# Performance work log

Measured on AMD Instinct MI355X. Metric: run time of the kernel, lower is better.

Reference implementation:

```python
import jax, jax.numpy as jnp
import numpy as np

D_MODEL = 768
D_STATE = 16
D_CONV = 4
EXPAND = 2
D_INNER = EXPAND * D_MODEL          # 1536
DT_RANK = max(1, D_MODEL // 16)     # 48
B, L = 2, 2048


def setup_inputs() -> dict:
    key = jax.random.key(0)
    ks = jax.random.split(key, 8)
    rn = lambda k, shape, scale: (jax.random.normal(k, shape, dtype=jnp.float32) * scale)
    A_init = jnp.broadcast_to(jnp.arange(1, D_STATE + 1, dtype=jnp.float32), (D_INNER, D_STATE))
    return {
        "x": rn(ks[0], (B, L, D_MODEL), 1.0),
        "in_proj_w": rn(ks[1], (2 * D_INNER, D_MODEL), 0.02),
        "conv_w": rn(ks[2], (D_INNER, 1, D_CONV), 0.2),
        "conv_b": jnp.zeros((D_INNER,), jnp.float32),
        "x_proj_w": rn(ks[3], (DT_RANK + 2 * D_STATE, D_INNER), 0.02),
        "dt_proj_w": rn(ks[4], (D_INNER, DT_RANK), 0.05),
        "dt_proj_b": rn(ks[5], (D_INNER,), 0.05),
        "A_log": jnp.log(A_init),
        "D_param": jnp.ones((D_INNER,), jnp.float32),
        "out_proj_w": rn(ks[6], (D_MODEL, D_INNER), 0.02),
        "ln_w": jnp.ones((D_MODEL,), jnp.float32),
        "ln_b": jnp.zeros((D_MODEL,), jnp.float32),
    }


def _layernorm(x, w, b, eps=1e-5):
    mu = x.mean(-1, keepdims=True)
    var = ((x - mu) ** 2).mean(-1, keepdims=True)
    return (x - mu) * jax.lax.rsqrt(var + eps) * w + b


def reference(x, in_proj_w, conv_w, conv_b, x_proj_w, dt_proj_w, dt_proj_b,
              A_log, D_param, out_proj_w, ln_w, ln_b):
    residual = x
    xn = _layernorm(x, ln_w, ln_b)
    xz = xn @ in_proj_w.T                      # [B,L,2*D_INNER]
    x_in, z = jnp.split(xz, 2, axis=-1)
    # depthwise causal conv (pad left d_conv-1, matching pad-both-then-slice)
    xc = jax.lax.conv_general_dilated(
        x_in.transpose(0, 2, 1), conv_w, (1,), [(D_CONV - 1, 0)],
        feature_group_count=D_INNER, dimension_numbers=("NCH", "OIH", "NCH"))
    xc = (xc + conv_b[None, :, None]).transpose(0, 2, 1)   # [B,L,D_INNER]
    xc = jax.nn.silu(xc)

    A = -jnp.exp(A_log)                        # [D_INNER, D_STATE]
    x_dbl = xc @ x_proj_w.T                    # [B,L,DT_RANK+2*D_STATE]
    dt, Bm, C = jnp.split(x_dbl, [DT_RANK, DT_RANK + D_STATE], axis=-1)
    delta = jax.nn.softplus(dt @ dt_proj_w.T + dt_proj_b)  # [B,L,D_INNER]
    deltaA = jnp.exp(jnp.einsum("bld,dn->bldn", delta, A))        # [B,L,D,N]
    deltaBx = jnp.einsum("bld,bln,bld->bldn", delta, Bm, xc)      # [B,L,D,N]

    def step(h, ins):
        dA, dBx, c = ins                       # [B,D,N],[B,D,N],[B,N]
        h = dA * h + dBx
        return h, jnp.einsum("bdn,bn->bd", h, c)

    h0 = jnp.zeros((x.shape[0], D_INNER, D_STATE), xc.dtype)
    _, ys = jax.lax.scan(step, h0, (deltaA.swapaxes(0, 1),
                                    deltaBx.swapaxes(0, 1),
                                    C.swapaxes(0, 1)))
    y = ys.swapaxes(0, 1) + xc * D_param       # [B,L,D_INNER]
    y = y * jax.nn.silu(z)
    return y @ out_proj_w.T + residual
```

## Files before the change

### kernel.cpp

```cpp
#include <hip/hip_runtime.h>
#include <hip/hip_bf16.h>
#include <math.h>

namespace {

typedef __hip_bfloat16 bf16;
typedef unsigned short u16;
typedef __bf16 bf8v __attribute__((ext_vector_type(8)));
typedef float f4v __attribute__((ext_vector_type(4)));
typedef short s8v __attribute__((ext_vector_type(8)));
typedef u16 u4v __attribute__((ext_vector_type(4)));

constexpr int Bb = 2;
constexpr int Ll = 2048;
constexpr int DM = 768;
constexpr int DI = 1536;
constexpr int DS = 16;
constexpr int RK = 48;
constexpr int XD = RK + 2 * DS;
constexpr int Mrows = Bb * Ll;
constexpr int NC = 32;
constexpr int CL = Ll / NC;
constexpr float LOG2E = 1.44269504f;

constexpr int NW1 = 2 * DI * DM;
constexpr int NWX = 128 * DI;
constexpr int NWD = DI * 64;
constexpr int NWO = DM * DI;
constexpr int NWC = DI * 4;
constexpr int NWCB = DI;

__device__ inline float b2f(bf16 v) { return __bfloat162float(v); }
__device__ inline bf16 f2b(float v) { return __float2bfloat16(v); }

union BfBits { bf16 h; u16 u; };
__device__ inline u16 f2u(float v) {
  BfBits bb; bb.h = __float2bfloat16(v); return bb.u;
}
__device__ inline float u2f(u16 u) {
  BfBits bb; bb.u = u; return b2f(bb.h);
}

__device__ inline float ldx(const void* p, size_t i, int bf) {
  if (bf) return __bfloat162float(((const bf16*)p)[i]);
  return ((const float*)p)[i];
}

__device__ inline void gload16(const void* g, u16* lds) {
  __builtin_amdgcn_global_load_lds(
      (__attribute__((address_space(1))) void*)g,
      (__attribute__((address_space(3))) void*)lds, 16, 0, 0);
}

__device__ inline int rperm(int d) {
  return (d & 56) | ((d ^ (d >> 3)) & 7);
}

__global__ void detect_kernel(const unsigned int* __restrict__ xw,
                              int* __restrict__ flag) {
  int t = threadIdx.x;
  unsigned int w = xw[t];
  unsigned int lo = w & 0xFFFFu;
  unsigned int ef = (lo >> 7) & 0xFFu;
  bool plaus = (lo == 0u) || (ef >= 104u && ef <= 136u);
  unsigned long long m = __ballot(plaus);
  if (t == 0) flag[0] = (__popcll(m) >= 48) ? 1 : 0;
}

__global__ __launch_bounds__(256) void convert_w1(
    const void* __restrict__ in_proj, const void* __restrict__ x_proj,
    const void* __restrict__ dt_proj, const void* __restrict__ conv_w,
    const void* __restrict__ conv_b,
    bf16* __restrict__ w_in, bf16* __restrict__ w_x, bf16* __restrict__ w_dt,
    bf16* __restrict__ dtA, bf16* __restrict__ w_cv, bf16* __restrict__ w_cb,
    const int* __restrict__ flagp) {
  int bf = flagp[0];
  int e = (blockIdx.x * 256 + threadIdx.x) * 4;
  if (e < NW1) {
    u4v v;
#pragma unroll
    for (int k = 0; k < 4; ++k) v[k] = f2u(ldx(in_proj, e + k, bf));
    *(u4v*)&w_in[e] = v;
    return;
  }
  e -= NW1;
  if (e < NWX) {
    int r = e / DI, c = e % DI;
    u4v v = {};
    if (r < 80) {
#pragma unroll
      for (int k = 0; k < 4; ++k) v[k] = f2u(ldx(x_proj, (size_t)r * DI + c + k, bf));
    }
    *(u4v*)&w_x[e] = v;
    return;
  }
  e -= NWX;
  if (e < NWD) {
    int r = e / 64, c = e % 64;
    u4v v = {};
#pragma unroll
    for (int k = 0; k < 4; ++k)
      if (c + k < RK) v[k] = f2u(ldx(dt_proj, (size_t)r * RK + c + k, bf));
    *(u4v*)&w_dt[e] = v;
    return;
  }
  e -= NWD;
  if (e < Mrows * 16) {
    int row = e / 16, col = RK + (e % 16);
    u4v v = {};
    *(u4v*)&dtA[(size_t)row * 64 + col] = v;
    return;
  }
  e -= Mrows * 16;
  if (e < NWC) {
    u4v v;
#pragma unroll
    for (int k = 0; k < 4; ++k) v[k] = f2u(ldx(conv_w, e + k, bf));
    *(u4v*)&w_cv[e] = v;
    return;
  }
  e -= NWC;
  if (e < NWCB) {
    u4v v;
#pragma unroll
    for (int k = 0; k < 4; ++k) v[k] = f2u(ldx(conv_b, e + k, bf));
    *(u4v*)&w_cb[e] = v;
  }
}

__global__ __launch_bounds__(256) void convert_w2(
    const void* __restrict__ out_proj, bf16* __restrict__ w_out,
    const int* __restrict__ flagp) {
  int bf = flagp[0];
  int e = (blockIdx.x * 256 + threadIdx.x) * 4;
  if (e >= NWO) return;
  u4v v;
#pragma unroll
  for (int k = 0; k < 4; ++k) v[k] = f2u(ldx(out_proj, e + k, bf));
  *(u4v*)&w_out[e] = v;
}

__global__ __launch_bounds__(256) void ln_kernel(
    const void* __restrict__ x, const void* __restrict__ w,
    const void* __restrict__ b, bf16* __restrict__ xn,
    const int* __restrict__ flagp) {
  int bf = flagp[0];
  int row = blockIdx.x;
  int t = threadIdx.x;
  float v[3];
  float s = 0.f, ss = 0.f;
#pragma unroll
  for (int i = 0; i < 3; ++i) {
    v[i] = ldx(x, (size_t)row * DM + t + i * 256, bf);
    s += v[i];
    ss += v[i] * v[i];
  }
#pragma unroll
  for (int off = 32; off; off >>= 1) {
    s += __shfl_down(s, off);
    ss += __shfl_down(ss, off);
  }
  __shared__ float sb[4], ssb[4];
  int wid = t >> 6, lid = t & 63;
  if (lid == 0) { sb[wid] = s; ssb[wid] = ss; }
  __syncthreads();
  if (t == 0) {
    sb[0] = sb[0] + sb[1] + sb[2] + sb[3];
    ssb[0] = ssb[0] + ssb[1] + ssb[2] + ssb[3];
  }
  __syncthreads();
  float mu = sb[0] * (1.f / DM);
  float var = ssb[0] * (1.f / DM) - mu * mu;
  float rs = rsqrtf(var + 1e-5f);
#pragma unroll
  for (int i = 0; i < 3; ++i) {
    int c = t + i * 256;
    xn[(size_t)row * DM + c] =
        f2b((v[i] - mu) * rs * ldx(w, c, bf) + ldx(b, c, bf));
  }
}

template <int EPI, int BM>
__global__ __launch_bounds__(256, 2) void gemm_gl(
    int M, int N, int klen,
    const bf16* __restrict__ A, int lda,
    const bf16* __restrict__ Bw, int ldb,
    void* __restrict__ Cv, void* __restrict__ Cv2, int ldc,
    const void* __restrict__ extra,
    const int* __restrict__ flagp) {
  constexpr int FI = BM / 32;
  __shared__ __align__(16) u16 As[2][BM * 32];
  __shared__ __align__(16) u16 Bs[2][128 * 32];
  int tid = threadIdx.x;
  int l = tid & 63, w = tid >> 6;
  int wr = w >> 1, wc = w & 1;
  int m0 = blockIdx.y * BM, n0 = blockIdx.x * 128;
  int kbeg = blockIdx.z * klen;
  int nt = klen / 64;
  int lr = l & 15, lk = (l >> 4) * 8;
  f4v acc[FI][4] = {};

  int srow = l >> 2, schunk = l & 3;

  for (int t = 0; t < nt; ++t) {
    __syncthreads();
#pragma unroll
    for (int h = 0; h < 2; ++h) {
      int k0 = kbeg + t * 64 + h * 32;
#pragma unroll
      for (int c = 0; c < BM / 64; ++c) {
        int seg = w + c * 4;
        int row = seg * 16 + srow;
        int gcol = k0 + ((schunk ^ ((row >> 1) & 3)) << 3);
        gload16(A + (size_t)(m0 + row) * lda + gcol, &As[h][seg * 512]);
      }
#pragma unroll
      for (int c = 0; c < 2; ++c) {
        int seg = w + c * 4;
        int row = seg * 16 + srow;
        int gcol = k0 + ((schunk ^ ((row >> 1) & 3)) << 3);
        gload16(Bw + (size_t)(n0 + row) * ldb + gcol, &Bs[h][seg * 512]);
      }
    }
    __syncthreads();
#pragma unroll
    for (int h = 0; h < 2; ++h) {
      bf8v af[FI], bfv[4];
#pragma unroll
      for (int i = 0; i < FI; ++i) {
        int row = wr * (BM / 2) + i * 16 + lr;
        af[i] = *(const bf8v*)&As[h][row * 32 + (((lk >> 3) ^ ((row >> 1) & 3)) << 3)];
      }
#pragma unroll
      for (int j = 0; j < 4; ++j) {
        int row = wc * 64 + j * 16 + lr;
        bfv[j] = *(const bf8v*)&Bs[h][row * 32 + (((lk >> 3) ^ ((row >> 1) & 3)) << 3)];
      }
#pragma unroll
      for (int i = 0; i < FI; ++i)
#pragma unroll
        for (int j = 0; j < 4; ++j)
          acc[i][j] = __builtin_amdgcn_mfma_f32_16x16x32_bf16(
              af[i], bfv[j], acc[i][j], 0, 0, 0);
    }
  }

  int bf = flagp[0];
  int lq = l >> 4;
  size_t pbase = (size_t)blockIdx.z * M * ldc;
#pragma unroll
  for (int i = 0; i < FI; ++i) {
#pragma unroll
    for (int j = 0; j < 4; ++j) {
      int nn = n0 + wc * 64 + j * 16 + lr;
      if (nn >= N) continue;
#pragma unroll
      for (int r = 0; r < 4; ++r) {
        int m = m0 + wr * (BM / 2) + i * 16 + lq * 4 + r;
        float v = acc[i][j][r];
        size_t ci = (size_t)m * ldc + nn;
        if (EPI == 0) {
          ((float*)Cv)[pbase + ci] = v;
        } else if (EPI == 1) {
          float tt = v + ldx(extra, nn, bf);
          float sp = (tt > 20.f) ? tt : log1pf(__expf(tt));
          ((bf16*)Cv)[ci] = f2b(sp);
        } else if (EPI == 4) {
          if (nn < DI) ((bf16*)Cv)[(size_t)m * DI + nn] = f2b(v);
          else ((bf16*)Cv2)[(size_t)m * DI + nn - DI] = f2b(v);
        }
      }
    }
  }
}

__global__ __launch_bounds__(256) void reduce_xdbl(
    const float* __restrict__ part, bf16* __restrict__ xdbl,
    bf16* __restrict__ dtA) {
  int idx = blockIdx.x * 256 + threadIdx.x;
  if (idx >= Mrows * XD) return;
  float s = 0.f;
#pragma unroll
  for (int k = 0; k < 8; ++k) s += part[(size_t)k * Mrows * XD + idx];
  bf16 v = f2b(s);
  xdbl[idx] = v;
  int col = idx % XD;
  if (col < RK) dtA[(size_t)(idx / XD) * 64 + col] = v;
}

__global__ __launch_bounds__(256) void reduce_out(
    const float* __restrict__ part, const void* __restrict__ x,
    float* __restrict__ out, const int* __restrict__ flagp) {
  int bf = flagp[0];
  int idx = blockIdx.x * 256 + threadIdx.x;
  if (idx >= Mrows * DM) return;
  out[idx] = part[idx] + part[(size_t)Mrows * DM + idx] + ldx(x, idx, bf);
}

__global__ __launch_bounds__(256) void conv_silu_kernel(
    const bf16* __restrict__ xin, const bf16* __restrict__ w_cv,
    const bf16* __restrict__ w_cb, bf16* __restrict__ xc) {
  int idx = blockIdx.x * 256 + threadIdx.x;
  if (idx >= Mrows * DI / 8) return;
  int d0 = (idx % (DI / 8)) * 8;
  int m = idx / (DI / 8);
  int l = m % Ll;
  s8v wv[4];
#pragma unroll
  for (int q = 0; q < 4; ++q)
    wv[q] = *(const s8v*)(w_cv + (size_t)d0 * 4 + q * 8);
  s8v cbv = *(const s8v*)(w_cb + d0);
  float acc[8];
#pragma unroll
  for (int k = 0; k < 8; ++k) acc[k] = u2f((u16)cbv[k]);
#pragma unroll
  for (int j = 0; j < 4; ++j) {
    int lj = l - 3 + j;
    if (lj < 0) continue;
    s8v xv = *(const s8v*)(xin + (size_t)(m - 3 + j) * DI + d0);
#pragma unroll
    for (int k = 0; k < 8; ++k)
      acc[k] += u2f((u16)wv[(k * 4 + j) >> 3][(k * 4 + j) & 7]) * u2f((u16)xv[k]);
  }
  s8v o;
#pragma unroll
  for (int k = 0; k < 8; ++k) {
    float v = acc[k] / (1.f + __expf(-acc[k]));
    o[k] = (short)f2u(v);
  }
  *(s8v*)(xc + (size_t)m * DI + d0) = o;
}

constexpr int TS = 72;

__global__ __launch_bounds__(256) void scan_p1(
    const bf16* __restrict__ delta, const bf16* __restrict__ xc,
    const bf16* __restrict__ xdbl, const void* __restrict__ A_log,
    float* __restrict__ ca, float* __restrict__ cb,
    const int* __restrict__ flagp) {
  int bf = flagp[0];
  int tid = threadIdx.x;
  int bx = blockIdx.x;
  int b = bx / NC, c = bx % NC;
  int dq = tid >> 2, n4 = tid & 3;
  int d0 = blockIdx.y * 64;
  int d = d0 + dq;
  __shared__ float Bsh[CL * 16];
  __shared__ __align__(16) u16 dT[64 * TS];
  __shared__ __align__(16) u16 xT[64 * TS];
  size_t base = (size_t)b * Ll + c * CL;
  {
    int e = tid * 4;
    int l = e >> 4, n = e & 15;
    size_t row = base + l;
    u4v v = *(const u4v*)((const u16*)xdbl + row * XD + RK + n);
#pragma unroll
    for (int k = 0; k < 4; ++k) Bsh[e + k] = u2f(v[k]);
  }
  {
    int lh = tid >> 3;
    int dd0 = (tid & 7) * 8;
    const u16* dg = (const u16*)delta + (base + 2 * lh) * DI + d0 + dd0;
    const u16* xg = (const u16*)xc + (base + 2 * lh) * DI + d0 + dd0;
    s8v d0v = *(const s8v*)dg;
    s8v d1v = *(const s8v*)(dg + DI);
    s8v x0v = *(const s8v*)xg;
    s8v x1v = *(const s8v*)(xg + DI);
#pragma unroll
    for (int k = 0; k < 8; ++k) {
      int rr = rperm(dd0 + k);
      unsigned int dw = (unsigned int)(u16)d0v[k] |
                        ((unsigned int)(u16)d1v[k] << 16);
      *(unsigned int*)&dT[rr * TS + 2 * lh] = dw;
      dw = (unsigned int)(u16)x0v[k] |
           ((unsigned int)(u16)x1v[k] << 16);
      *(unsigned int*)&xT[rr * TS + 2 * lh] = dw;
    }
  }
  __syncthreads();
  int rq = rperm(dq);
  float An2[4], h[4] = {};
  float sdv = 0.f;
#pragma unroll
  for (int k = 0; k < 4; ++k)
    An2[k] = -__expf(ldx(A_log, (size_t)d * DS + n4 * 4 + k, bf)) * LOG2E;
  for (int l0 = 0; l0 < CL; l0 += 8) {
    s8v dvv = *(const s8v*)&dT[rq * TS + l0];
    s8v xvv = *(const s8v*)&xT[rq * TS + l0];
    float dv[8], xcv[8];
#pragma unroll
    for (int k2 = 0; k2 < 8; ++k2) {
      dv[k2] = u2f((u16)dvv[k2]);
      xcv[k2] = u2f((u16)xvv[k2]);
    }
#pragma unroll
    for (int j = 0; j < 8; ++j) {
      f4v bv = *(const f4v*)&Bsh[(l0 + j) * 16 + n4 * 4];
      float dx = dv[j] * xcv[j];
      sdv += dv[j];
#pragma unroll
      for (int k = 0; k < 4; ++k) {
        float dA = exp2f(dv[j] * An2[k]);
        h[k] = dA * h[k] + dx * bv[k];
      }
    }
  }
  size_t cbase = ((size_t)bx * DI + d) * 16 + n4 * 4;
  f4v av, hv;
#pragma unroll
  for (int k = 0; k < 4; ++k) {
    av[k] = exp2f(sdv * An2[k]);
    hv[k] = h[k];
  }
  *(f4v*)&ca[cbase] = av;
  *(f4v*)&cb[cbase] = hv;
}

__global__ __launch_bounds__(256) void scan_p2(
    const float* __restrict__ ca, float* __restrict__ cb) {
  int tid = threadIdx.x;
  int bx = blockIdx.x;
  int b = bx / (DI / 64);
  int d = (bx % (DI / 64)) * 64 + (tid >> 2);
  int n4 = tid & 3;
  size_t off = (size_t)d * 16 + n4 * 4;
  f4v h = {};
  for (int c = 0; c < NC; ++c) {
    size_t cbase = (size_t)(b * NC + c) * DI * 16 + off;
    f4v av = *(const f4v*)&ca[cbase];
    f4v bv = *(const f4v*)&cb[cbase];
    f4v hv = h;
#pragma unroll
    for (int k = 0; k < 4; ++k) h[k] = av[k] * h[k] + bv[k];
    *(f4v*)&cb[cbase] = hv;
  }
}

__global__ __launch_bounds__(256) void scan_p3(
    bf16* dy, const bf16* __restrict__ xc,
    const bf16* __restrict__ xdbl, const bf16* __restrict__ z,
    const void* __restrict__ A_log, const void* __restrict__ Dp,
    const float* __restrict__ cb, const int* __restrict__ flagp) {
  int bf = flagp[0];
  int tid = threadIdx.x;
  int bx = blockIdx.x;
  int b = bx / NC, c = bx % NC;
  int dq = tid >> 2, n4 = tid & 3;
  int d0 = blockIdx.y * 64;
  int d = d0 + dq;
  __shared__ float BCsh[CL * 32];
  __shared__ __align__(16) u16 dT[64 * TS];
  __shared__ __align__(16) u16 xT[64 * TS];
  size_t base = (size_t)b * Ll + c * CL;
  {
    int e = tid * 8;
    int l = e >> 5, j = e & 31;
    size_t row = base + l;
    s8v v = *(const s8v*)((const u16*)xdbl + row * XD + RK + j);
#pragma unroll
    for (int k = 0; k < 8; ++k) BCsh[e + k] = u2f((u16)v[k]);
  }
  {
    int lh = tid >> 3;
    int dd0 = (tid & 7) * 8;
    const u16* dg = (const u16*)dy + (base + 2 * lh) * DI + d0 + dd0;
    const u16* xg = (const u16*)xc + (base + 2 * lh) * DI + d0 + dd0;
    s8v d0v = *(const s8v*)dg;
    s8v d1v = *(const s8v*)(dg + DI);
    s8v x0v = *(const s8v*)xg;
    s8v x1v = *(const s8v*)(xg + DI);
#pragma unroll
    for (int k = 0; k < 8; ++k) {
      int rr = rperm(dd0 + k);
      unsigned int dw = (unsigned int)(u16)d0v[k] |
                        ((unsigned int)(u16)d1v[k] << 16);
      *(unsigned int*)&dT[rr * TS + 2 * lh] = dw;
      dw = (unsigned int)(u16)x0v[k] |
           ((unsigned int)(u16)x1v[k] << 16);
      *(unsigned int*)&xT[rr * TS + 2 * lh] = dw;
    }
  }
  __syncthreads();
  int rq = rperm(dq);
  float An2[4], h[4];
  size_t cbase = ((size_t)bx * DI + d) * 16 + n4 * 4;
  {
    f4v hv = *(const f4v*)&cb[cbase];
#pragma unroll
    for (int k = 0; k < 4; ++k) h[k] = hv[k];
  }
#pragma unroll
  for (int k = 0; k < 4; ++k)
    An2[k] = -__expf(ldx(A_log, (size_t)d * DS + n4 * 4 + k, bf)) * LOG2E;
  float Dv = ldx(Dp, d, bf);
  bf16* dp = dy + base * DI + d;
  const bf16* zp = z + base * DI + d;
  for (int l0 = 0; l0 < CL; l0 += 8) {
    s8v dvv = *(const s8v*)&dT[rq * TS + l0];
    s8v xvv = *(const s8v*)&xT[rq * TS + l0];
    float dv[8], xcv[8];
#pragma unroll
    for (int k2 = 0; k2 < 8; ++k2) {
      dv[k2] = u2f((u16)dvv[k2]);
      xcv[k2] = u2f((u16)xvv[k2]);
    }
    float zg0 = b2f(zp[(size_t)(l0 + n4) * DI]);
    float zg1 = b2f(zp[(size_t)(l0 + 4 + n4) * DI]);
#pragma unroll
    for (int half = 0; half < 2; ++half) {
      float accK = 0.f, xg = 0.f;
#pragma unroll
      for (int jj = 0; jj < 4; ++jj) {
        int j = half * 4 + jj;
        f4v bv = *(const f4v*)&BCsh[(l0 + j) * 32 + n4 * 4];
        f4v cv = *(const f4v*)&BCsh[(l0 + j) * 32 + 16 + n4 * 4];
        float dx = dv[j] * xcv[j];
        float acc = 0.f;
#pragma unroll
        for (int k = 0; k < 4; ++k) {
          float dA = exp2f(dv[j] * An2[k]);
          h[k] = dA * h[k] + dx * bv[k];
          acc += h[k] * cv[k];
        }
        acc += __shfl_xor(acc, 1, 4);
        acc += __shfl_xor(acc, 2, 4);
        if (n4 == jj) { accK = acc; xg = xcv[j]; }
      }
      float zg = half ? zg1 : zg0;
      float yv = (accK + xg * Dv) * (zg / (1.f + __expf(-zg)));
      dp[(size_t)(l0 + half * 4 + n4) * DI] = f2b(yv);
    }
  }
}

}

extern "C" void kernel_launch(void* const* d_in, const int* in_sizes, int n_in,
                              void* d_out, int out_size, void* d_ws, size_t ws_size,
                              hipStream_t stream) {
  const void* x        = d_in[0];
  const void* in_proj  = d_in[1];
  const void* conv_w   = d_in[2];
  const void* conv_b   = d_in[3];
  const void* x_proj   = d_in[4];
  const void* dt_proj  = d_in[5];
  const void* dt_b     = d_in[6];
  const void* A_log    = d_in[7];
  const void* Dp       = d_in[8];
  const void* out_proj = d_in[9];
  const void* ln_w     = d_in[10];
  const void* ln_b     = d_in[11];
  float* out = (float*)d_out;

  char* wsc = (char*)d_ws;
  int* flag = (int*)wsc;
  bf16* xn   = (bf16*)(wsc + 256);
  bf16* buf1 = xn + (size_t)Mrows * DM;
  bf16* z    = buf1 + (size_t)Mrows * DI;
  bf16* xc   = z + (size_t)Mrows * DI;
  bf16* xdbl = xc + (size_t)Mrows * DI;
  float* carry_b = (float*)(xdbl + (size_t)Mrows * XD);
  bf16* dtA = (bf16*)((float*)carry_b + (size_t)Bb * NC * DI * 16);
  bf16* w_in = dtA + (size_t)Mrows * 64;
  bf16* w_cv = w_in + (size_t)NW1;
  bf16* w_cb = w_cv + (size_t)NWC;
  float* carry_a = (float*)xn;
  bf16* w_out = (bf16*)xn;
  bf16* w_x  = (bf16*)carry_b;
  bf16* w_dt = w_x + (size_t)NWX;
  float* part8 = (float*)buf1;
  float* part2 = (float*)z;

  detect_kernel<<<1, 64, 0, stream>>>((const unsigned int*)x, flag);
  {
    int quads = (NW1 + NWX + NWD + Mrows * 16 + NWC + NWCB) / 4;
    convert_w1<<<(quads + 255) / 256, 256, 0, stream>>>(
        in_proj, x_proj, dt_proj, conv_w, conv_b,
        w_in, w_x, w_dt, dtA, w_cv, w_cb, flag);
  }
  ln_kernel<<<Mrows, 256, 0, stream>>>(x, ln_w, ln_b, xn, flag);
  gemm_gl<4, 128><<<dim3(2 * DI / 128, Mrows / 128, 1), 256, 0, stream>>>(
      Mrows, 2 * DI, DM, xn, DM, w_in, DM, buf1, z, DI, nullptr, flag);
  conv_silu_kernel<<<(Mrows * DI / 8) / 256, 256, 0, stream>>>(
      buf1, w_cv, w_cb, xc);
  gemm_gl<0, 64><<<dim3(1, Mrows / 64, 8), 256, 0, stream>>>(
      Mrows, XD, DI / 8, xc, DI, w_x, DI, part8, nullptr, XD, nullptr, flag);
  reduce_xdbl<<<(Mrows * XD + 255) / 256, 256, 0, stream>>>(part8, xdbl, dtA);
  gemm_gl<1, 64><<<dim3(DI / 128, Mrows / 64, 1), 256, 0, stream>>>(
      Mrows, DI, 64, dtA, 64, w_dt, 64, buf1, nullptr, DI, dt_b, flag);
  scan_p1<<<dim3(Bb * NC, DI / 64), 256, 0, stream>>>(
      buf1, xc, xdbl, A_log, carry_a, carry_b, flag);
  scan_p2<<<Bb * (DI / 64), 256, 0, stream>>>(carry_a, carry_b);
  scan_p3<<<dim3(Bb * NC, DI / 64), 256, 0, stream>>>(
      buf1, xc, xdbl, z, A_log, Dp, carry_b, flag);
  convert_w2<<<(NWO / 4 + 255) / 256, 256, 0, stream>>>(out_proj, w_out, flag);
  gemm_gl<0, 64><<<dim3(DM / 128, Mrows / 64, 2), 256, 0, stream>>>(
      Mrows, DM, DI / 2, buf1, DI, w_out, DI, part2, nullptr, DM, nullptr, flag);
  reduce_out<<<(Mrows * DM + 255) / 256, 256, 0, stream>>>(part2, x, out, flag);
}
```

Before: 221.8 us.

## Fold chunk-carry prefix scan into scan_p3 and raise GEMM occupancy hint

Removes the separate scan_p2 kernel; each scan_p3 block now recomputes its own incoming state by serially combining carries from all preceding chunks, overlapping that with the shared-memory staging before the barrier. This saves a kernel launch and a serial pass over the carries, at the cost of redundant global reads that grow with the chunk index (up to 31 chunks). It also hoists the B/C shared-memory loads out of the inner recurrence loops in both scan kernels, and raises the GEMM launch-bounds minimum from 2 to 3 blocks per SIMD, which may cause register spills.

Result: slower. 229.7 us (+3.6%).

```diff
diff --git a/kernel.cpp b/kernel.cpp
--- a/kernel.cpp
+++ b/kernel.cpp
@@ -181,7 +181,7 @@
 }
 
 template <int EPI, int BM>
-__global__ __launch_bounds__(256, 2) void gemm_gl(
+__global__ __launch_bounds__(256, 3) void gemm_gl(
     int M, int N, int klen,
     const bf16* __restrict__ A, int lda,
     const bf16* __restrict__ Bw, int ldb,
@@ -393,15 +393,18 @@
       dv[k2] = u2f((u16)dvv[k2]);
       xcv[k2] = u2f((u16)xvv[k2]);
     }
+    f4v bvv[8];
+#pragma unroll
+    for (int j = 0; j < 8; ++j)
+      bvv[j] = *(const f4v*)&Bsh[(l0 + j) * 16 + n4 * 4];
 #pragma unroll
     for (int j = 0; j < 8; ++j) {
-      f4v bv = *(const f4v*)&Bsh[(l0 + j) * 16 + n4 * 4];
       float dx = dv[j] * xcv[j];
       sdv += dv[j];
 #pragma unroll
       for (int k = 0; k < 4; ++k) {
         float dA = exp2f(dv[j] * An2[k]);
-        h[k] = dA * h[k] + dx * bv[k];
+        h[k] = dA * h[k] + dx * bvv[j][k];
       }
     }
   }
@@ -414,33 +417,14 @@
   }
   *(f4v*)&ca[cbase] = av;
   *(f4v*)&cb[cbase] = hv;
-}
-
-__global__ __launch_bounds__(256) void scan_p2(
-    const float* __restrict__ ca, float* __restrict__ cb) {
-  int tid = threadIdx.x;
-  int bx = blockIdx.x;
-  int b = bx / (DI / 64);
-  int d = (bx % (DI / 64)) * 64 + (tid >> 2);
-  int n4 = tid & 3;
-  size_t off = (size_t)d * 16 + n4 * 4;
-  f4v h = {};
-  for (int c = 0; c < NC; ++c) {
-    size_t cbase = (size_t)(b * NC + c) * DI * 16 + off;
-    f4v av = *(const f4v*)&ca[cbase];
-    f4v bv = *(const f4v*)&cb[cbase];
-    f4v hv = h;
-#pragma unroll
-    for (int k = 0; k < 4; ++k) h[k] = av[k] * h[k] + bv[k];
-    *(f4v*)&cb[cbase] = hv;
-  }
 }
 
 __global__ __launch_bounds__(256) void scan_p3(
     bf16* dy, const bf16* __restrict__ xc,
     const bf16* __restrict__ xdbl, const bf16* __restrict__ z,
     const void* __restrict__ A_log, const void* __restrict__ Dp,
-    const float* __restrict__ cb, const int* __restrict__ flagp) {
+    const float* __restrict__ ca, const float* __restrict__ cb,
+    const int* __restrict__ flagp) {
   int bf = flagp[0];
   int tid = threadIdx.x;
   int bx = blockIdx.x;
@@ -480,15 +464,18 @@
       *(unsigned int*)&xT[rr * TS + 2 * lh] = dw;
     }
   }
+  float h[4] = {};
+  size_t coff = (size_t)d * 16 + n4 * 4;
+  for (int cc = 0; cc < c; ++cc) {
+    size_t cbase2 = (size_t)(b * NC + cc) * DI * 16 + coff;
+    f4v av = *(const f4v*)&ca[cbase2];
+    f4v bv = *(const f4v*)&cb[cbase2];
+#pragma unroll
+    for (int k = 0; k < 4; ++k) h[k] = av[k] * h[k] + bv[k];
+  }
   __syncthreads();
   int rq = rperm(dq);
-  float An2[4], h[4];
-  size_t cbase = ((size_t)bx * DI + d) * 16 + n4 * 4;
-  {
-    f4v hv = *(const f4v*)&cb[cbase];
-#pragma unroll
-    for (int k = 0; k < 4; ++k) h[k] = hv[k];
-  }
+  float An2[4];
 #pragma unroll
   for (int k = 0; k < 4; ++k)
     An2[k] = -__expf(ldx(A_log, (size_t)d * DS + n4 * 4 + k, bf)) * LOG2E;
@@ -508,19 +495,24 @@
     float zg1 = b2f(zp[(size_t)(l0 + 4 + n4) * DI]);
 #pragma unroll
     for (int half = 0; half < 2; ++half) {
-      float accK = 0.f, xg = 0.f;
+      f4v bvv[4], cvv[4];
 #pragma unroll
       for (int jj = 0; jj < 4; ++jj) {
         int j = half * 4 + jj;
-        f4v bv = *(const f4v*)&BCsh[(l0 + j) * 32 + n4 * 4];
-        f4v cv = *(const f4v*)&BCsh[(l0 + j) * 32 + 16 + n4 * 4];
+        bvv[jj] = *(const f4v*)&BCsh[(l0 + j) * 32 + n4 * 4];
+        cvv[jj] = *(const f4v*)&BCsh[(l0 + j) * 32 + 16 + n4 * 4];
+      }
+      float accK = 0.f, xg = 0.f;
+#pragma unroll
+      for (int jj = 0; jj < 4; ++jj) {
+        int j = half * 4 + jj;
         float dx = dv[j] * xcv[j];
         float acc = 0.f;
 #pragma unroll
         for (int k = 0; k < 4; ++k) {
           float dA = exp2f(dv[j] * An2[k]);
-          h[k] = dA * h[k] + dx * bv[k];
-          acc += h[k] * cv[k];
+          h[k] = dA * h[k] + dx * bvv[jj][k];
+          acc += h[k] * cvv[jj][k];
         }
         acc += __shfl_xor(acc, 1, 4);
         acc += __shfl_xor(acc, 2, 4);
@@ -590,9 +582,8 @@
       Mrows, DI, 64, dtA, 64, w_dt, 64, buf1, nullptr, DI, dt_b, flag);
   scan_p1<<<dim3(Bb * NC, DI / 64), 256, 0, stream>>>(
       buf1, xc, xdbl, A_log, carry_a, carry_b, flag);
-  scan_p2<<<Bb * (DI / 64), 256, 0, stream>>>(carry_a, carry_b);
   scan_p3<<<dim3(Bb * NC, DI / 64), 256, 0, stream>>>(
-      buf1, xc, xdbl, z, A_log, Dp, carry_b, flag);
+      buf1, xc, xdbl, z, A_log, Dp, carry_a, carry_b, flag);
   convert_w2<<<(NWO / 4 + 255) / 256, 256, 0, stream>>>(out_proj, w_out, flag);
   gemm_gl<0, 64><<<dim3(DM / 128, Mrows / 64, 2), 256, 0, stream>>>(
       Mrows, DM, DI / 2, buf1, DI, w_out, DI, part2, nullptr, DM, nullptr, flag);
```
